# Kernel optimization log

Hardware: AMD Instinct MI355X
Metric: run time of the kernel (lower is better)

## Reference

```python
import jax, jax.numpy as jnp
import numpy as np
from jax import lax

B, C, D, H, W = 2, 64, 16, 16, 16  # n = D*H*W = 4096; conv output length = n-2 = 4094
K = 3  # conv kernel size, dilation=2, padding=1


def setup_inputs() -> dict:
    key = jax.random.key(0)
    k1, k2, k3 = jax.random.split(key, 3)
    x = jax.random.normal(k1, (B, C, D, H, W), dtype=jnp.float32)
    # Conv1d params: weight [out_ch, in_ch, k], bias [out_ch]; PyTorch default init scale
    fan_in = C * K
    bound = 1.0 / np.sqrt(fan_in)
    conv_w = jax.random.uniform(k2, (C, C, K), jnp.float32, -bound, bound)
    conv_b = jax.random.uniform(k3, (C,), jnp.float32, -bound, bound)
    return {"x": x, "conv_w": conv_w, "conv_b": conv_b}


def _dspa(x, conv_w, conv_b):
    b, c, d, h, w = x.shape
    x1 = x.reshape(b, c, -1)  # [b, c, n]
    # dilated Conv1d: kernel=3, stride=1, padding=1, dilation=2 -> length n-2
    x2 = lax.conv_general_dilated(
        x1, conv_w,
        window_strides=(1,), padding=[(1, 1)], rhs_dilation=(2,),
        dimension_numbers=("NCH", "OIH", "NCH"),
    ) + conv_b[None, :, None]  # [b, c, n-2]
    # scores = bmm(x1^T, x2): [b, n, n-2]
    scores = jnp.einsum("bcn,bcm->bnm", x1, x2)
    # torch nn.Softmax() (dim=None) on a 3D tensor resolves to dim=0 (legacy behavior)
    x3 = jax.nn.softmax(scores, axis=0)  # [b, n, n-2]
    # x4 = bmm(x2, x3^T): [b, c, n]
    x4 = jnp.einsum("bcm,bnm->bcn", x2, x3)
    out = x1 + x4
    return out.reshape(b, c, d, h, w)


def reference(x, conv_w, conv_b):
    return _dspa(x, conv_w, conv_b)
```

## Files before the change

kernel.cpp:

```cpp
#include <hip/hip_runtime.h>

typedef unsigned short u16;
typedef unsigned int u32;
typedef __attribute__((ext_vector_type(8))) short bf16x8;
typedef __attribute__((ext_vector_type(4))) float f32x4;

#define NJ 4094

__device__ __forceinline__ u16 f2bf(float f) {
  union { float f; unsigned u; } v;
  v.f = f;
  unsigned r = v.u + 0x7fffu + ((v.u >> 16) & 1u);
  return (u16)(r >> 16);
}

__device__ __forceinline__ u32 pk_bf(float a, float b) {
  u32 ua = __float_as_uint(a) + 0x8000u;
  u32 ub = __float_as_uint(b) + 0x8000u;
  return __builtin_amdgcn_perm(ub, ua, 0x07060302u);
}

template <bool WRITE_OUT>
__global__ __launch_bounds__(256) void conv_kernel(
    const float* __restrict__ x, const float* __restrict__ w,
    const float* __restrict__ bias, u16* __restrict__ x2n, u16* __restrict__ x2T,
    u16* __restrict__ x1T, float* __restrict__ out) {
  __shared__ float xs[64 * 36];
  __shared__ float wl[64 * 64 * 3];
  const int b = blockIdx.x >> 7, jt = blockIdx.x & 127;
  const int t = threadIdx.x;
  for (int idx = t; idx < 64 * 36; idx += 256) {
    int i = idx / 36, p = idx - i * 36;
    int jg = jt * 32 - 1 + p;
    float v = 0.f;
    if (jg >= 0 && jg < 4096) v = x[(b * 64 + i) * 4096 + jg];
    xs[idx] = v;
  }
  for (int idx = t; idx < 64 * 64 * 3; idx += 256) {
    int tap = idx % 3, ci = idx / 3;
    int c = ci >> 6, i = ci & 63;
    wl[(i * 64 + c) * 3 + tap] = w[idx];
  }
  __syncthreads();
  for (int idx = t; idx < 32 * 64; idx += 256) {
    int il = idx >> 6, c = idx & 63;
    float v = xs[c * 36 + il + 1];
    x1T[(b * 4096 + jt * 32 + il) * 64 + c] = f2bf(b ? -v : v);
  }
  if (WRITE_OUT) {
    for (int idx = t; idx < 64 * 32; idx += 256) {
      int i = idx >> 5, k = idx & 31;
      out[(b * 64 + i) * 4096 + jt * 32 + k] = xs[i * 36 + k + 1];
    }
  }
  const int c = t & 63, jsub = t >> 6;
  float acc[8];
  float bv = bias[c];
#pragma unroll
  for (int k = 0; k < 8; k++) acc[k] = bv;
  for (int i = 0; i < 64; i++) {
    float w0 = wl[(i * 64 + c) * 3 + 0];
    float w1 = wl[(i * 64 + c) * 3 + 1];
    float w2 = wl[(i * 64 + c) * 3 + 2];
    const float* xr = &xs[i * 36 + jsub * 8];
#pragma unroll
    for (int k = 0; k < 8; k++)
      acc[k] += w0 * xr[k] + w1 * xr[k + 2] + w2 * xr[k + 4];
  }
#pragma unroll
  for (int k = 0; k < 8; k++) {
    int jg = jt * 32 + jsub * 8 + k;
    float v = (jg < NJ) ? acc[k] : 0.f;
    u16 hv = f2bf(v);
    x2n[(b * 64 + c) * 4096 + jg] = hv;
    x2T[(b * 4096 + jg) * 64 + c] = hv;
  }
}

template <bool ATOMIC>
__global__ __launch_bounds__(256, 4) void fused_kernel(
    const u16* __restrict__ x1T_g, const u16* __restrict__ x2n_g,
    const u16* __restrict__ x2T_g, float* __restrict__ part_g,
    float* __restrict__ out) {
  __shared__ u16 P[2][2 * 64 * 72];
  const int t = threadIdx.x;
  const int wave = t >> 6, lane = t & 63;
  const int q = lane >> 4, ln = lane & 15;
  const int i0 = blockIdx.x * 64;
  const int jc = blockIdx.y;

  bf16x8 b1[2][4][2];
#pragma unroll
  for (int b = 0; b < 2; b++)
#pragma unroll
    for (int ist = 0; ist < 4; ist++)
#pragma unroll
      for (int kc = 0; kc < 2; kc++)
        b1[b][ist][kc] = *(const bf16x8*)&x1T_g[(b * 4096 + i0 + ist * 16 + ln) * 64 + kc * 32 + q * 8];

  f32x4 acc[2][4];
#pragma unroll
  for (int a = 0; a < 2; a++)
#pragma unroll
    for (int bq = 0; bq < 4; bq++) acc[a][bq] = (f32x4){0.f, 0.f, 0.f, 0.f};

  const int b2 = wave >> 1, cs2 = (wave & 1) * 2;

  for (int jt = jc * 4; jt < jc * 4 + 4; jt++) {
    const int j0 = jt * 64;
    u16* Ps = P[jt & 1];
    f32x4 ps[4];
#pragma unroll
    for (int ist = 0; ist < 4; ist++) ps[ist] = (f32x4){0.f, 0.f, 0.f, 0.f};
#pragma unroll
    for (int b = 0; b < 2; b++)
#pragma unroll
      for (int kc = 0; kc < 2; kc++) {
        bf16x8 af = *(const bf16x8*)&x2T_g[(b * 4096 + j0 + wave * 16 + ln) * 64 + kc * 32 + q * 8];
#pragma unroll
        for (int ist = 0; ist < 4; ist++)
          ps[ist] = __builtin_amdgcn_mfma_f32_16x16x32_bf16(af, b1[b][ist][kc], ps[ist], 0, 0, 0);
      }
#pragma unroll
    for (int ist = 0; ist < 4; ist++) {
      float p0[4], p1[4];
#pragma unroll
      for (int r = 0; r < 4; r++) {
        float e = __expf(-ps[ist][r]);
        p0[r] = __builtin_amdgcn_rcpf(1.f + e);
        p1[r] = 1.f - p0[r];
      }
      uint2 o0 = make_uint2(pk_bf(p0[0], p0[1]), pk_bf(p0[2], p0[3]));
      uint2 o1 = make_uint2(pk_bf(p1[0], p1[1]), pk_bf(p1[2], p1[3]));
      *(uint2*)&Ps[(0 + ist * 16 + ln) * 72 + wave * 16 + q * 4] = o0;
      *(uint2*)&Ps[(64 + ist * 16 + ln) * 72 + wave * 16 + q * 4] = o1;
    }
    __syncthreads();
#pragma unroll
    for (int kc = 0; kc < 2; kc++) {
      bf16x8 af2[2], pb[4];
#pragma unroll
      for (int cst = 0; cst < 2; cst++)
        af2[cst] = *(const bf16x8*)&x2n_g[(b2 * 64 + (cs2 + cst) * 16 + ln) * 4096 + j0 + kc * 32 + q * 8];
#pragma unroll
      for (int ist = 0; ist < 4; ist++)
        pb[ist] = *(const bf16x8*)&Ps[(b2 * 64 + ist * 16 + ln) * 72 + kc * 32 + q * 8];
#pragma unroll
      for (int cst = 0; cst < 2; cst++)
#pragma unroll
        for (int ist = 0; ist < 4; ist++)
          acc[cst][ist] =
              __builtin_amdgcn_mfma_f32_16x16x32_bf16(af2[cst], pb[ist], acc[cst][ist], 0, 0, 0);
    }
  }
  if (ATOMIC) {
#pragma unroll
    for (int cst = 0; cst < 2; cst++)
#pragma unroll
      for (int ist = 0; ist < 4; ist++)
#pragma unroll
        for (int r = 0; r < 4; r++) {
          int c = (cs2 + cst) * 16 + q * 4 + r;
          int ii = i0 + ist * 16 + ln;
          unsafeAtomicAdd(&out[(b2 * 64 + c) * 4096 + ii], acc[cst][ist][r]);
        }
  } else {
    __syncthreads();
    float* scr = (float*)P;
#pragma unroll
    for (int cst = 0; cst < 2; cst++)
#pragma unroll
      for (int ist = 0; ist < 4; ist++)
#pragma unroll
        for (int r = 0; r < 4; r++) {
          int c = (cs2 + cst) * 16 + q * 4 + r;
          scr[(b2 * 64 + c) * 68 + ist * 16 + ln] = acc[cst][ist][r];
        }
    __syncthreads();
#pragma unroll
    for (int rep = 0; rep < 8; rep++) {
      int idx = rep * 256 + t;
      int crow = idx >> 4, il4 = idx & 15;
      float4 v = *(float4*)&scr[crow * 68 + il4 * 4];
      int b = crow >> 6, c = crow & 63;
      *(float4*)&part_g[(((jc * 2 + b) * 64 + c) << 12) + i0 + il4 * 4] = v;
    }
  }
}

__global__ __launch_bounds__(256) void reduce_kernel(
    const float4* __restrict__ x, const float4* __restrict__ part,
    float4* __restrict__ out) {
  int i = blockIdx.x * 256 + threadIdx.x;
  float4 s = x[i];
#pragma unroll
  for (int jc = 0; jc < 16; jc++) {
    float4 p = part[jc * 131072 + i];
    s.x += p.x; s.y += p.y; s.z += p.z; s.w += p.w;
  }
  out[i] = s;
}

extern "C" void kernel_launch(void* const* d_in, const int* in_sizes, int n_in,
                              void* d_out, int out_size, void* d_ws, size_t ws_size,
                              hipStream_t stream) {
  const float* x = (const float*)d_in[0];
  const float* w = (const float*)d_in[1];
  const float* bias = (const float*)d_in[2];
  float* out = (float*)d_out;
  u16* x2n = (u16*)d_ws;
  u16* x2T = x2n + 2 * 64 * 4096;
  u16* x1T = x2T + 2 * 64 * 4096;
  float* part = (float*)(x1T + 2 * 64 * 4096);

  const size_t need = 3u * (2 * 64 * 4096 * 2) + 16u * 2 * 64 * 4096 * 4;
  dim3 grid(64, 16);
  if (ws_size >= need) {
    conv_kernel<false><<<256, 256, 0, stream>>>(x, w, bias, x2n, x2T, x1T, out);
    fused_kernel<false><<<grid, 256, 0, stream>>>(x1T, x2n, x2T, part, out);
    reduce_kernel<<<512, 256, 0, stream>>>((const float4*)x, (const float4*)part, (float4*)out);
  } else {
    conv_kernel<true><<<256, 256, 0, stream>>>(x, w, bias, x2n, x2T, x1T, out);
    fused_kernel<true><<<grid, 256, 0, stream>>>(x1T, x2n, x2T, nullptr, out);
  }
}
```

Baseline: 109.9 us.

## Merge conv, attention and reduction into one cooperative kernel with grid syncs

Replaces the three-launch pipeline (conv, fused attention, reduce) with a single cooperative kernel that uses grid-wide syncs between phases. The conv phase is split across all 1024 blocks with smaller tiles, and the partial sums are stored as bf16 instead of fp32, halving the partial-buffer traffic. The aim is to remove launch gaps and underused conv blocks. The cost is two grid barriers, a co-residency requirement of 1024 blocks, and extra rounding error from the bf16 partials.

```diff
diff --git a/kernel.cpp b/kernel.cpp
--- a/kernel.cpp
+++ b/kernel.cpp
@@ -1,4 +1,7 @@
 #include <hip/hip_runtime.h>
+#include <hip/hip_cooperative_groups.h>
+
+namespace cg = cooperative_groups;
 
 typedef unsigned short u16;
 typedef unsigned int u32;
@@ -20,8 +23,169 @@
   return __builtin_amdgcn_perm(ub, ua, 0x07060302u);
 }
 
-template <bool WRITE_OUT>
-__global__ __launch_bounds__(256) void conv_kernel(
+__global__ __launch_bounds__(256, 4) void mono_kernel(
+    const float* __restrict__ x, const float* __restrict__ w,
+    const float* __restrict__ bias, u16* __restrict__ x2n, u16* __restrict__ x2T,
+    u16* __restrict__ x1T, u16* __restrict__ part, float* __restrict__ out) {
+  __shared__ __align__(16) char smem[36864];
+  const int t = threadIdx.x;
+  const int flat = blockIdx.y * 64 + blockIdx.x;
+
+  {
+    float* xs = (float*)smem;
+    float* wl = xs + 64 * 20;
+    const int b = flat >> 9, jt = (flat >> 1) & 255, ch = flat & 1;
+    for (int idx = t; idx < 64 * 20; idx += 256) {
+      int i = idx / 20, p = idx - i * 20;
+      int jg = jt * 16 - 1 + p;
+      xs[idx] = (jg >= 0 && jg < 4096) ? x[(b * 64 + i) * 4096 + jg] : 0.f;
+    }
+    for (int idx = t; idx < 32 * 64 * 3; idx += 256) {
+      int tap = idx % 3, rest = idx / 3;
+      int co = rest >> 6, i = rest & 63;
+      wl[(i * 32 + co) * 3 + tap] = w[((ch * 32 + co) * 64 + i) * 3 + tap];
+    }
+    __syncthreads();
+    if (ch == 0) {
+      for (int idx = t; idx < 16 * 64; idx += 256) {
+        int ii = idx >> 6, ic = idx & 63;
+        float v = xs[ic * 20 + ii + 1];
+        x1T[(b * 4096 + jt * 16 + ii) * 64 + ic] = f2bf(b ? -v : v);
+      }
+    }
+    const int co = t & 31, jsub = t >> 5;
+    const int c = ch * 32 + co;
+    float a0 = bias[c], a1 = a0;
+    for (int i = 0; i < 64; i++) {
+      float w0 = wl[(i * 32 + co) * 3 + 0];
+      float w1 = wl[(i * 32 + co) * 3 + 1];
+      float w2 = wl[(i * 32 + co) * 3 + 2];
+      const float* xr = &xs[i * 20 + jsub * 2];
+      a0 += w0 * xr[0] + w1 * xr[2] + w2 * xr[4];
+      a1 += w0 * xr[1] + w1 * xr[3] + w2 * xr[5];
+    }
+    int jg0 = jt * 16 + jsub * 2;
+    u16 h0 = f2bf(jg0 < NJ ? a0 : 0.f);
+    u16 h1 = f2bf(jg0 + 1 < NJ ? a1 : 0.f);
+    x2n[(b * 64 + c) * 4096 + jg0] = h0;
+    x2n[(b * 64 + c) * 4096 + jg0 + 1] = h1;
+    x2T[(b * 4096 + jg0) * 64 + c] = h0;
+    x2T[(b * 4096 + jg0 + 1) * 64 + c] = h1;
+  }
+  cg::this_grid().sync();
+
+  {
+    u16 (*P)[2 * 64 * 72] = (u16(*)[2 * 64 * 72])smem;
+    const int wave = t >> 6, lane = t & 63;
+    const int q = lane >> 4, ln = lane & 15;
+    const int i0 = blockIdx.x * 64;
+    const int jc = blockIdx.y;
+
+    bf16x8 b1[2][4][2];
+#pragma unroll
+    for (int b = 0; b < 2; b++)
+#pragma unroll
+      for (int ist = 0; ist < 4; ist++)
+#pragma unroll
+        for (int kc = 0; kc < 2; kc++)
+          b1[b][ist][kc] = *(const bf16x8*)&x1T[(b * 4096 + i0 + ist * 16 + ln) * 64 + kc * 32 + q * 8];
+
+    f32x4 acc[2][4];
+#pragma unroll
+    for (int a = 0; a < 2; a++)
+#pragma unroll
+      for (int bq = 0; bq < 4; bq++) acc[a][bq] = (f32x4){0.f, 0.f, 0.f, 0.f};
+
+    const int b2 = wave >> 1, cs2 = (wave & 1) * 2;
+
+    for (int jt = jc * 4; jt < jc * 4 + 4; jt++) {
+      const int j0 = jt * 64;
+      u16* Ps = P[jt & 1];
+      f32x4 ps[4];
+#pragma unroll
+      for (int ist = 0; ist < 4; ist++) ps[ist] = (f32x4){0.f, 0.f, 0.f, 0.f};
+#pragma unroll
+      for (int b = 0; b < 2; b++)
+#pragma unroll
+        for (int kc = 0; kc < 2; kc++) {
+          bf16x8 af = *(const bf16x8*)&x2T[(b * 4096 + j0 + wave * 16 + ln) * 64 + kc * 32 + q * 8];
+#pragma unroll
+          for (int ist = 0; ist < 4; ist++)
+            ps[ist] = __builtin_amdgcn_mfma_f32_16x16x32_bf16(af, b1[b][ist][kc], ps[ist], 0, 0, 0);
+        }
+#pragma unroll
+      for (int ist = 0; ist < 4; ist++) {
+        float p0[4], p1[4];
+#pragma unroll
+        for (int r = 0; r < 4; r++) {
+          float e = __expf(-ps[ist][r]);
+          p0[r] = __builtin_amdgcn_rcpf(1.f + e);
+          p1[r] = 1.f - p0[r];
+        }
+        uint2 o0 = make_uint2(pk_bf(p0[0], p0[1]), pk_bf(p0[2], p0[3]));
+        uint2 o1 = make_uint2(pk_bf(p1[0], p1[1]), pk_bf(p1[2], p1[3]));
+        *(uint2*)&Ps[(0 + ist * 16 + ln) * 72 + wave * 16 + q * 4] = o0;
+        *(uint2*)&Ps[(64 + ist * 16 + ln) * 72 + wave * 16 + q * 4] = o1;
+      }
+      __syncthreads();
+#pragma unroll
+      for (int kc = 0; kc < 2; kc++) {
+        bf16x8 af2[2], pb[4];
+#pragma unroll
+        for (int cst = 0; cst < 2; cst++)
+          af2[cst] = *(const bf16x8*)&x2n[(b2 * 64 + (cs2 + cst) * 16 + ln) * 4096 + j0 + kc * 32 + q * 8];
+#pragma unroll
+        for (int ist = 0; ist < 4; ist++)
+          pb[ist] = *(const bf16x8*)&Ps[(b2 * 64 + ist * 16 + ln) * 72 + kc * 32 + q * 8];
+#pragma unroll
+        for (int cst = 0; cst < 2; cst++)
+#pragma unroll
+          for (int ist = 0; ist < 4; ist++)
+            acc[cst][ist] =
+                __builtin_amdgcn_mfma_f32_16x16x32_bf16(af2[cst], pb[ist], acc[cst][ist], 0, 0, 0);
+      }
+    }
+    __syncthreads();
+    float* scr = (float*)smem;
+#pragma unroll
+    for (int cst = 0; cst < 2; cst++)
+#pragma unroll
+      for (int ist = 0; ist < 4; ist++)
+#pragma unroll
+        for (int r = 0; r < 4; r++) {
+          int c = (cs2 + cst) * 16 + q * 4 + r;
+          scr[(b2 * 64 + c) * 68 + ist * 16 + ln] = acc[cst][ist][r];
+        }
+    __syncthreads();
+#pragma unroll
+    for (int rep = 0; rep < 4; rep++) {
+      int idx = rep * 256 + t;
+      int crow = idx >> 3, ck = idx & 7;
+      const float* s = &scr[crow * 68 + ck * 8];
+      u32 w0 = pk_bf(s[0], s[1]), w1 = pk_bf(s[2], s[3]);
+      u32 w2 = pk_bf(s[4], s[5]), w3 = pk_bf(s[6], s[7]);
+      int b = crow >> 6, c = crow & 63;
+      u16* dst = &part[(size_t)((jc * 2 + b) * 64 + c) * 4096 + i0 + ck * 8];
+      *(uint4*)dst = make_uint4(w0, w1, w2, w3);
+    }
+  }
+  cg::this_grid().sync();
+
+  {
+    int id = flat * 256 + t;
+    int off = id * 2;
+    float2 s = *(const float2*)&x[off];
+#pragma unroll
+    for (int j = 0; j < 16; j++) {
+      u32 pw = *(const u32*)&part[(size_t)j * 524288 + off];
+      s.x += __uint_as_float(pw << 16);
+      s.y += __uint_as_float(pw & 0xffff0000u);
+    }
+    *(float2*)&out[off] = s;
+  }
+}
+
+__global__ __launch_bounds__(256) void conv_fb_kernel(
     const float* __restrict__ x, const float* __restrict__ w,
     const float* __restrict__ bias, u16* __restrict__ x2n, u16* __restrict__ x2T,
     u16* __restrict__ x1T, float* __restrict__ out) {
@@ -32,9 +196,7 @@
   for (int idx = t; idx < 64 * 36; idx += 256) {
     int i = idx / 36, p = idx - i * 36;
     int jg = jt * 32 - 1 + p;
-    float v = 0.f;
-    if (jg >= 0 && jg < 4096) v = x[(b * 64 + i) * 4096 + jg];
-    xs[idx] = v;
+    xs[idx] = (jg >= 0 && jg < 4096) ? x[(b * 64 + i) * 4096 + jg] : 0.f;
   }
   for (int idx = t; idx < 64 * 64 * 3; idx += 256) {
     int tap = idx % 3, ci = idx / 3;
@@ -47,11 +209,9 @@
     float v = xs[c * 36 + il + 1];
     x1T[(b * 4096 + jt * 32 + il) * 64 + c] = f2bf(b ? -v : v);
   }
-  if (WRITE_OUT) {
-    for (int idx = t; idx < 64 * 32; idx += 256) {
-      int i = idx >> 5, k = idx & 31;
-      out[(b * 64 + i) * 4096 + jt * 32 + k] = xs[i * 36 + k + 1];
-    }
+  for (int idx = t; idx < 64 * 32; idx += 256) {
+    int i = idx >> 5, k = idx & 31;
+    out[(b * 64 + i) * 4096 + jt * 32 + k] = xs[i * 36 + k + 1];
   }
   const int c = t & 63, jsub = t >> 6;
   float acc[8];
@@ -70,25 +230,21 @@
 #pragma unroll
   for (int k = 0; k < 8; k++) {
     int jg = jt * 32 + jsub * 8 + k;
-    float v = (jg < NJ) ? acc[k] : 0.f;
-    u16 hv = f2bf(v);
+    u16 hv = f2bf(jg < NJ ? acc[k] : 0.f);
     x2n[(b * 64 + c) * 4096 + jg] = hv;
     x2T[(b * 4096 + jg) * 64 + c] = hv;
   }
 }
 
-template <bool ATOMIC>
-__global__ __launch_bounds__(256, 4) void fused_kernel(
+__global__ __launch_bounds__(256, 4) void fused_fb_kernel(
     const u16* __restrict__ x1T_g, const u16* __restrict__ x2n_g,
-    const u16* __restrict__ x2T_g, float* __restrict__ part_g,
-    float* __restrict__ out) {
+    const u16* __restrict__ x2T_g, float* __restrict__ out) {
   __shared__ u16 P[2][2 * 64 * 72];
   const int t = threadIdx.x;
   const int wave = t >> 6, lane = t & 63;
   const int q = lane >> 4, ln = lane & 15;
   const int i0 = blockIdx.x * 64;
   const int jc = blockIdx.y;
-
   bf16x8 b1[2][4][2];
 #pragma unroll
   for (int b = 0; b < 2; b++)
@@ -97,15 +253,12 @@
 #pragma unroll
       for (int kc = 0; kc < 2; kc++)
         b1[b][ist][kc] = *(const bf16x8*)&x1T_g[(b * 4096 + i0 + ist * 16 + ln) * 64 + kc * 32 + q * 8];
-
   f32x4 acc[2][4];
 #pragma unroll
   for (int a = 0; a < 2; a++)
 #pragma unroll
     for (int bq = 0; bq < 4; bq++) acc[a][bq] = (f32x4){0.f, 0.f, 0.f, 0.f};
-
   const int b2 = wave >> 1, cs2 = (wave & 1) * 2;
-
   for (int jt = jc * 4; jt < jc * 4 + 4; jt++) {
     const int j0 = jt * 64;
     u16* Ps = P[jt & 1];
@@ -153,52 +306,16 @@
               __builtin_amdgcn_mfma_f32_16x16x32_bf16(af2[cst], pb[ist], acc[cst][ist], 0, 0, 0);
     }
   }
-  if (ATOMIC) {
-#pragma unroll
-    for (int cst = 0; cst < 2; cst++)
-#pragma unroll
-      for (int ist = 0; ist < 4; ist++)
-#pragma unroll
-        for (int r = 0; r < 4; r++) {
-          int c = (cs2 + cst) * 16 + q * 4 + r;
-          int ii = i0 + ist * 16 + ln;
-          unsafeAtomicAdd(&out[(b2 * 64 + c) * 4096 + ii], acc[cst][ist][r]);
-        }
-  } else {
-    __syncthreads();
-    float* scr = (float*)P;
-#pragma unroll
-    for (int cst = 0; cst < 2; cst++)
-#pragma unroll
-      for (int ist = 0; ist < 4; ist++)
-#pragma unroll
-        for (int r = 0; r < 4; r++) {
-          int c = (cs2 + cst) * 16 + q * 4 + r;
-          scr[(b2 * 64 + c) * 68 + ist * 16 + ln] = acc[cst][ist][r];
-        }
-    __syncthreads();
-#pragma unroll
-    for (int rep = 0; rep < 8; rep++) {
-      int idx = rep * 256 + t;
-      int crow = idx >> 4, il4 = idx & 15;
-      float4 v = *(float4*)&scr[crow * 68 + il4 * 4];
-      int b = crow >> 6, c = crow & 63;
-      *(float4*)&part_g[(((jc * 2 + b) * 64 + c) << 12) + i0 + il4 * 4] = v;
-    }
-  }
-}
-
-__global__ __launch_bounds__(256) void reduce_kernel(
-    const float4* __restrict__ x, const float4* __restrict__ part,
-    float4* __restrict__ out) {
-  int i = blockIdx.x * 256 + threadIdx.x;
-  float4 s = x[i];
-#pragma unroll
-  for (int jc = 0; jc < 16; jc++) {
-    float4 p = part[jc * 131072 + i];
-    s.x += p.x; s.y += p.y; s.z += p.z; s.w += p.w;
-  }
-  out[i] = s;
+#pragma unroll
+  for (int cst = 0; cst < 2; cst++)
+#pragma unroll
+    for (int ist = 0; ist < 4; ist++)
+#pragma unroll
+      for (int r = 0; r < 4; r++) {
+        int c = (cs2 + cst) * 16 + q * 4 + r;
+        int ii = i0 + ist * 16 + ln;
+        unsafeAtomicAdd(&out[(b2 * 64 + c) * 4096 + ii], acc[cst][ist][r]);
+      }
 }
 
 extern "C" void kernel_launch(void* const* d_in, const int* in_sizes, int n_in,
@@ -211,16 +328,17 @@
   u16* x2n = (u16*)d_ws;
   u16* x2T = x2n + 2 * 64 * 4096;
   u16* x1T = x2T + 2 * 64 * 4096;
-  float* part = (float*)(x1T + 2 * 64 * 4096);
-
-  const size_t need = 3u * (2 * 64 * 4096 * 2) + 16u * 2 * 64 * 4096 * 4;
+  u16* part = x1T + 2 * 64 * 4096;
+
+  const size_t need = 3u * (2 * 64 * 4096 * 2) + 16u * 2 * 64 * 4096 * 2;
+  if (ws_size >= need) {
+    void* args[] = {(void*)&x, (void*)&w, (void*)&bias, (void*)&x2n,
+                    (void*)&x2T, (void*)&x1T, (void*)&part, (void*)&out};
+    hipError_t e = hipLaunchCooperativeKernel((const void*)mono_kernel, dim3(64, 16),
+                                              dim3(256), args, 0, stream);
+    if (e == hipSuccess) return;
+  }
+  conv_fb_kernel<<<256, 256, 0, stream>>>(x, w, bias, x2n, x2T, x1T, out);
   dim3 grid(64, 16);
-  if (ws_size >= need) {
-    conv_kernel<false><<<256, 256, 0, stream>>>(x, w, bias, x2n, x2T, x1T, out);
-    fused_kernel<false><<<grid, 256, 0, stream>>>(x1T, x2n, x2T, part, out);
-    reduce_kernel<<<512, 256, 0, stream>>>((const float4*)x, (const float4*)part, (float4*)out);
-  } else {
-    conv_kernel<true><<<256, 256, 0, stream>>>(x, w, bias, x2n, x2T, x1T, out);
-    fused_kernel<true><<<grid, 256, 0, stream>>>(x1T, x2n, x2T, nullptr, out);
-  }
-}
+  fused_fb_kernel<<<grid, 256, 0, stream>>>(x1T, x2n, x2T, out);
+}
```

Result: slower. 341.6 us (+210.9%).
